# Performance work log

Hardware: AMD Instinct MI355X
Metric: run time of the kernel (lower is better)

## Reference

```python
import jax, jax.numpy as jnp
import numpy as np

B, P, G = 16, 16000, 256          # images, RPN proposals, gt boxes per image
S = 512                           # batch_size_per_image
POS_FRAC = 0.25
FG_T, BG_T = 0.5, 0.5             # fg/bg IoU thresholds
NUM_CLASSES = 91
BOX_W = jnp.array([10.0, 10.0, 5.0, 5.0], jnp.float32)  # box_coder weights
BETA = 1.0 / 9.0                  # smooth_l1 beta


def _make_boxes(k, n, img=800.0, maxwh=200.0):
    k1, k2 = jax.random.split(k)
    xy = jax.random.uniform(k1, (B, n, 2)) * img
    wh = jax.random.uniform(k2, (B, n, 2)) * maxwh + 1.0
    return jnp.concatenate([xy, xy + wh], -1)


def setup_inputs() -> dict:
    key = jax.random.key(0)
    ks = jax.random.split(key, 6)
    proposals = _make_boxes(ks[0], P)
    gt_boxes = _make_boxes(ks[1], G)
    gt_labels = jax.random.randint(ks[2], (B, G), 1, NUM_CLASSES)
    gt_thetas = jax.random.uniform(ks[3], (B, G)) * np.pi
    class_logits = jax.random.normal(ks[4], (B * S, NUM_CLASSES))
    box_regression = jax.random.normal(ks[5], (B * S, NUM_CLASSES * 5))
    return dict(class_logits=class_logits, box_regression=box_regression,
                proposals=proposals, gt_boxes=gt_boxes,
                gt_thetas=gt_thetas, gt_labels=gt_labels)


def _box_iou(a, b):
    # a: [G,4] gt, b: [M,4] proposals -> [G,M]
    area_a = (a[:, 2] - a[:, 0]) * (a[:, 3] - a[:, 1])
    area_b = (b[:, 2] - b[:, 0]) * (b[:, 3] - b[:, 1])
    lt = jnp.maximum(a[:, None, :2], b[None, :, :2])
    rb = jnp.minimum(a[:, None, 2:], b[None, :, 2:])
    wh = jnp.clip(rb - lt, 0.0)
    inter = wh[..., 0] * wh[..., 1]
    return inter / (area_a[:, None] + area_b[None, :] - inter)


def _encode(ref, prop):
    pw = prop[:, 2] - prop[:, 0]; ph = prop[:, 3] - prop[:, 1]
    px = prop[:, 0] + 0.5 * pw;   py = prop[:, 1] + 0.5 * ph
    gw = ref[:, 2] - ref[:, 0];   gh = ref[:, 3] - ref[:, 1]
    gx = ref[:, 0] + 0.5 * gw;    gy = ref[:, 1] + 0.5 * gh
    t = jnp.stack([(gx - px) / pw, (gy - py) / ph,
                   jnp.log(gw / pw), jnp.log(gh / ph)], 1)
    return t * BOX_W[None, :]


def _select_training_samples(props, gtb, gtl, gtt):
    # add_gt_proposals
    props_all = jnp.concatenate([props, gtb], 0)        # [P+G,4]
    # assign_targets_to_proposals (Matcher, allow_low_quality=False)
    iou = _box_iou(gtb, props_all)                      # [G,P+G]
    vals = iou.max(0)
    matches = iou.argmax(0)                             # clamped matched idxs
    below = vals < BG_T
    between = (vals >= BG_T) & (vals < FG_T)
    lbl = gtl[matches]
    lbl = jnp.where(below, 0, lbl)      # background
    lbl = jnp.where(between, -1, lbl)   # ignored
    # BalancedPositiveNegativeSampler (deterministic first-k variant)
    pos = lbl > 0
    neg = lbl == 0
    n_pos = jnp.minimum(pos.sum(), int(S * POS_FRAC))
    sel_pos = pos & (jnp.cumsum(pos) <= n_pos)
    sel_neg = neg & (jnp.cumsum(neg) <= (S - n_pos))
    mask = sel_pos | sel_neg
    sampled = jnp.argsort((~mask).astype(jnp.int32), stable=True)[:S]  # sorted selected idxs
    props_s = props_all[sampled]
    lbl_s = lbl[sampled]
    m = matches[sampled]
    reg = _encode(gtb[m], props_s)                       # [S,4]
    reg_t = jnp.concatenate([reg, gtt[m][:, None]], 1)   # append theta -> [S,5]
    return lbl_s, reg_t


def _fastrcnn_loss(class_logits, box_regression, labels, reg_targets):
    N = class_logits.shape[0]
    logp = jax.nn.log_softmax(class_logits, -1)
    cls_loss = -jnp.take_along_axis(logp, labels[:, None], 1).mean()
    br = box_regression.reshape(N, -1, 5)
    idx = jnp.broadcast_to(labels[:, None, None], (N, 1, 5))
    pred = jnp.take_along_axis(br, idx, axis=1)[:, 0, :]
    d = pred - reg_targets
    ad = jnp.abs(d)
    sl1 = jnp.where(ad < BETA, 0.5 * d * d / BETA, ad - 0.5 * BETA)
    pos = (labels > 0).astype(sl1.dtype)
    box_loss = jnp.sum(sl1 * pos[:, None]) / N
    return jnp.stack([cls_loss, box_loss])


def reference(class_logits, box_regression, proposals, gt_boxes, gt_thetas, gt_labels):
    labels, reg_t = jax.vmap(_select_training_samples)(proposals, gt_boxes, gt_labels, gt_thetas)
    labels = labels.reshape(-1)
    reg_t = reg_t.reshape(-1, 5)
    return _fastrcnn_loss(class_logits, box_regression, labels, reg_t)
```

## Files before the change

### kernel.cpp

```cpp
#include <hip/hip_runtime.h>

#define NB 16
#define NP 16000
#define NG 256
#define NM (NP + NG)
#define NSTRIP 254
#define NS 512
#define NCLS 91
#define SL1_BETA (1.0f/9.0f)
#define MATCHX 64
#define STATSX 4

__global__ __launch_bounds__(256) void k1_kernel(
    const float4* __restrict__ props4,
    const float4* __restrict__ gt4,
    const int*    __restrict__ gt_labels,
    const float*  __restrict__ logits,
    unsigned int* __restrict__ posinfo,
    float*        __restrict__ stats)
{
    const int b    = blockIdx.y;
    const int bx   = blockIdx.x;
    const int tid  = threadIdx.x;
    const int lane = tid & 63;
    const int wid  = tid >> 6;

    if (bx >= MATCHX) {
        const int sid = (bx - MATCHX) * NB + b;
        for (int rr = 0; rr < 32; ++rr) {
            const int r = sid * 128 + wid * 32 + rr;
            const float* row = logits + (size_t)r * NCLS;
            float a = (lane < NCLS)      ? row[lane]      : -3.0e38f;
            float c = (lane + 64 < NCLS) ? row[lane + 64] : -3.0e38f;
            float mx = fmaxf(a, c);
            #pragma unroll
            for (int o = 32; o; o >>= 1) mx = fmaxf(mx, __shfl_xor(mx, o, 64));
            float ss = 0.0f;
            if (lane < NCLS)      ss += expf(a - mx);
            if (lane + 64 < NCLS) ss += expf(c - mx);
            #pragma unroll
            for (int o = 32; o; o >>= 1) ss += __shfl_xor(ss, o, 64);
            if (lane == 0) stats[r] = mx + logf(ss);
        }
        return;
    }

    __shared__ float4 gbox[NG];
    __shared__ float  gar[NG];

    {
        const float4 v = gt4[(size_t)b * NG + tid];
        gbox[tid] = v;
        gar[tid]  = (v.z - v.x) * (v.w - v.y);
    }
    __syncthreads();

    const int j = bx * 256 + tid;
    if (j >= NM) return;

    const float4 pb = (j < NP) ? props4[(size_t)b * NP + j]
                               : gt4[(size_t)b * NG + (j - NP)];
    const float ap = (pb.z - pb.x) * (pb.w - pb.y);

    unsigned qm[8];
    int qcnt = 0, gf = 0;
    #pragma unroll
    for (int w = 0; w < 8; ++w) {
        unsigned m = 0;
        #pragma unroll
        for (int t = 0; t < 32; ++t) {
            const int g = w * 32 + t;
            const float4 gb = gbox[g];
            const float  ga = gar[g];
            float lx = fmaxf(gb.x, pb.x), ly = fmaxf(gb.y, pb.y);
            float rx = fminf(gb.z, pb.z), ry = fminf(gb.w, pb.w);
            float ww = fmaxf(rx - lx, 0.0f), hh = fmaxf(ry - ly, 0.0f);
            float inter = ww * hh;
            float tt = ga + ap;
            if (fmaf(inter, 3.0f, -tt) >= 0.0f) m |= (1u << t);
        }
        qm[w] = m;
        if (qcnt == 0 && m) gf = w * 32 + (__ffs(m) - 1);
        qcnt += __popc(m);
    }

    unsigned info = 0;
    if (qcnt > 0) {
        int gstar = gf;
        if (qcnt > 1) {
            float ib = -1.0f, ub = 1.0f; gstar = 0;
            #pragma unroll
            for (int w = 0; w < 8; ++w) {
                unsigned m = qm[w];
                while (m) {
                    int t = __ffs(m) - 1; m &= m - 1;
                    int g = w * 32 + t;
                    const float4 gb = gbox[g];
                    float lx = fmaxf(gb.x, pb.x), ly = fmaxf(gb.y, pb.y);
                    float rx = fminf(gb.z, pb.z), ry = fminf(gb.w, pb.w);
                    float ww = fmaxf(rx - lx, 0.0f), hh = fmaxf(ry - ly, 0.0f);
                    float inter = ww * hh;
                    float u = (gar[g] + ap) - inter;
                    if (inter * ub > ib * u) { ib = inter; ub = u; gstar = g; }
                }
            }
        }
        info = ((unsigned)gstar << 16) | (unsigned)gt_labels[b * NG + gstar];
    }
    posinfo[(size_t)b * NM + j] = info;
}

__global__ __launch_bounds__(256) void k2_kernel(
    const float4* __restrict__ props4,
    const float4* __restrict__ gt4,
    const float*  __restrict__ gt_thetas,
    const unsigned int* __restrict__ posinfo,
    const float*  __restrict__ logits,
    const float*  __restrict__ boxreg,
    const float*  __restrict__ stats,
    float2* __restrict__ partials)
{
    __shared__ int sampled[NS];
    __shared__ int wsum[4];

    const int b    = blockIdx.x;
    const int tid  = threadIdx.x;
    const int lane = tid & 63;
    const int wid  = tid >> 6;
    const unsigned* P = posinfo + (size_t)b * NM;
    const int base = tid * 64;

    unsigned long long pm = 0ull;
    int cn = 0;
    if (tid < NSTRIP) {
        const uint4* Pv = reinterpret_cast<const uint4*>(P + base);
        #pragma unroll
        for (int q = 0; q < 16; ++q) {
            uint4 v = Pv[q];
            int e = q * 4;
            if (v.x) pm |= 1ull << (e + 0);
            if (v.y) pm |= 1ull << (e + 1);
            if (v.z) pm |= 1ull << (e + 2);
            if (v.w) pm |= 1ull << (e + 3);
        }
        cn = 64 - __popcll(pm);
    }
    int cp = (tid < NSTRIP) ? __popcll(pm) : 0;
    int val  = (cp << 16) | cn;
    int incl = val;
    #pragma unroll
    for (int off = 1; off < 64; off <<= 1) {
        int u = __shfl_up(incl, off, 64);
        if (lane >= off) incl += u;
    }
    if (lane == 63) wsum[wid] = incl;
    __syncthreads();
    int wbase = 0;
    #pragma unroll
    for (int w = 0; w < 4; ++w) if (w < wid) wbase += wsum[w];
    int tot  = wsum[0] + wsum[1] + wsum[2] + wsum[3];
    int excl = wbase + incl - val;
    int rp = excl >> 16, rn = excl & 0xffff;
    int posT = tot >> 16, negT = tot & 0xffff;
    int np = posT < 128 ? posT : 128;
    int nn = NS - np; if (nn > negT) nn = negT;

    if (tid < NSTRIP) {
        #pragma unroll 4
        for (int e = 0; e < 64; ++e) {
            int idx = base + e;
            if ((pm >> e) & 1ull) {
                if (rp < np) sampled[rp + (rn < nn ? rn : nn)] = idx;
                rp++;
            } else {
                if (rn < nn) sampled[rn + (rp < np ? rp : np)] = idx;
                rn++;
            }
        }
    }
    __syncthreads();
    if (tid == 0 && np + nn < NS) {
        int cpp = 0, cnn = 0, i = np + nn;
        for (int idx = 0; idx < NM && i < NS; ++idx) {
            bool p = P[idx] != 0;
            bool sel;
            if (p) { sel = cpp < np; cpp++; } else { sel = cnn < nn; cnn++; }
            if (!sel) sampled[i++] = idx;
        }
    }
    __syncthreads();

    float cls_acc = 0.0f, box_acc = 0.0f;
    #pragma unroll
    for (int it = 0; it < 2; ++it) {
        const int i = tid + it * 256;
        const int r = b * NS + i;
        const int idx = sampled[i];
        const unsigned info = P[idx];
        int lbl = 0;
        if (info) lbl = info & 0xffff;
        cls_acc += stats[r] - logits[(size_t)r * NCLS + lbl];
        if (info) {
            const int m = info >> 16;
            float4 pv = (idx < NP) ? props4[(size_t)b * NP + idx]
                                   : gt4[(size_t)b * NG + (idx - NP)];
            float4 rv = gt4[(size_t)b * NG + m];
            float pw = pv.z - pv.x, ph = pv.w - pv.y;
            float px = pv.x + 0.5f * pw, py = pv.y + 0.5f * ph;
            float gw = rv.z - rv.x, gh = rv.w - rv.y;
            float gx = rv.x + 0.5f * gw, gy = rv.y + 0.5f * gh;
            float o0 = 10.0f * (gx - px) / pw;
            float o1 = 10.0f * (gy - py) / ph;
            float o2 = 5.0f * logf(gw / pw);
            float o3 = 5.0f * logf(gh / ph);
            float o4 = gt_thetas[b * NG + m];
            const float* pr = boxreg + (size_t)r * (NCLS * 5) + lbl * 5;
            float tg[5] = { o0, o1, o2, o3, o4 };
            #pragma unroll
            for (int k = 0; k < 5; ++k) {
                float d  = pr[k] - tg[k];
                float ad = fabsf(d);
                box_acc += (ad < SL1_BETA) ? 0.5f * d * d / SL1_BETA
                                           : ad - 0.5f * SL1_BETA;
            }
        }
    }
    #pragma unroll
    for (int o = 32; o; o >>= 1) {
        cls_acc += __shfl_xor(cls_acc, o, 64);
        box_acc += __shfl_xor(box_acc, o, 64);
    }
    __shared__ float cc[4], bb[4];
    if (lane == 0) { cc[wid] = cls_acc; bb[wid] = box_acc; }
    __syncthreads();
    if (tid == 0)
        partials[b] = make_float2(cc[0] + cc[1] + cc[2] + cc[3],
                                  bb[0] + bb[1] + bb[2] + bb[3]);
}

__global__ void final_kernel(const float2* __restrict__ partials,
                             float* __restrict__ out)
{
    const int tid = threadIdx.x;
    float2 v = (tid < NB) ? partials[tid] : make_float2(0.f, 0.f);
    float c = v.x, bx = v.y;
    #pragma unroll
    for (int o = 32; o; o >>= 1) {
        c  += __shfl_xor(c, o, 64);
        bx += __shfl_xor(bx, o, 64);
    }
    if (tid == 0) {
        const float invN = 1.0f / (float)(NB * NS);
        out[0] = c * invN;
        out[1] = bx * invN;
    }
}

extern "C" void kernel_launch(void* const* d_in, const int* in_sizes, int n_in,
                              void* d_out, int out_size, void* d_ws, size_t ws_size,
                              hipStream_t stream)
{
    const float* class_logits   = (const float*)d_in[0];
    const float* box_regression = (const float*)d_in[1];
    const float4* props4        = (const float4*)d_in[2];
    const float4* gt4           = (const float4*)d_in[3];
    const float* gt_thetas      = (const float*)d_in[4];
    const int*   gt_labels      = (const int*)d_in[5];
    float* out = (float*)d_out;

    char* ws = (char*)d_ws;
    unsigned int* posinfo = (unsigned int*)ws;
    char* pend = ws + (((size_t)NB * NM * 4 + 255) & ~255ull);
    float* stats = (float*)pend;
    float2* partials = (float2*)(pend + (((size_t)NB * NS * 4 + 255) & ~255ull));

    hipLaunchKernelGGL(k1_kernel, dim3(MATCHX + STATSX, NB), dim3(256), 0, stream,
                       props4, gt4, gt_labels, class_logits, posinfo, stats);
    hipLaunchKernelGGL(k2_kernel, dim3(NB), dim3(256), 0, stream,
                       props4, gt4, gt_thetas, posinfo, class_logits,
                       box_regression, stats, partials);
    hipLaunchKernelGGL(final_kernel, dim3(1), dim3(64), 0, stream, partials, out);
}
```

Baseline: 60.29 us.

## Process two proposals per thread in IoU matching to reuse gt box loads

Each thread in the matching kernel now handles two proposals (A and B), so each gt box read from LDS is shared by two IoU evaluations. The grid shrinks by half (MATCHX 64->32). The gt area is recomputed inline instead of kept in a shared array, and the inner loop goes from full unroll to unroll 4. This is meant to cut LDS traffic and block count per proposal, at the cost of more registers, possible lower occupancy, and fewer blocks to spread across CUs.

```diff
diff --git a/kernel.cpp b/kernel.cpp
--- a/kernel.cpp
+++ b/kernel.cpp
@@ -8,7 +8,7 @@
 #define NS 512
 #define NCLS 91
 #define SL1_BETA (1.0f/9.0f)
-#define MATCHX 64
+#define MATCHX 32
 #define STATSX 4
 
 __global__ __launch_bounds__(256) void k1_kernel(
@@ -46,68 +46,108 @@
     }
 
     __shared__ float4 gbox[NG];
-    __shared__ float  gar[NG];
-
-    {
-        const float4 v = gt4[(size_t)b * NG + tid];
-        gbox[tid] = v;
-        gar[tid]  = (v.z - v.x) * (v.w - v.y);
-    }
-    __syncthreads();
-
-    const int j = bx * 256 + tid;
-    if (j >= NM) return;
-
-    const float4 pb = (j < NP) ? props4[(size_t)b * NP + j]
-                               : gt4[(size_t)b * NG + (j - NP)];
-    const float ap = (pb.z - pb.x) * (pb.w - pb.y);
-
-    unsigned qm[8];
-    int qcnt = 0, gf = 0;
+
+    gbox[tid] = gt4[(size_t)b * NG + tid];
+    __syncthreads();
+
+    const int jA = bx * 512 + tid;
+    const int jB = jA + 256;
+    const bool vB = (jB < NM);
+
+    const float4 pA = (jA < NP) ? props4[(size_t)b * NP + jA] : gbox[jA - NP];
+    float4 pB = make_float4(0.f, 0.f, 0.f, 0.f);
+    if (vB) pB = (jB < NP) ? props4[(size_t)b * NP + jB] : gbox[jB - NP];
+    const float apA = (pA.z - pA.x) * (pA.w - pA.y);
+    const float apB = (pB.z - pB.x) * (pB.w - pB.y);
+
+    unsigned qmA[8], qmB[8];
+    int qcA = 0, qcB = 0, gfA = 0, gfB = 0;
     #pragma unroll
     for (int w = 0; w < 8; ++w) {
-        unsigned m = 0;
-        #pragma unroll
+        unsigned mA = 0, mB = 0;
+        #pragma unroll 4
         for (int t = 0; t < 32; ++t) {
-            const int g = w * 32 + t;
-            const float4 gb = gbox[g];
-            const float  ga = gar[g];
-            float lx = fmaxf(gb.x, pb.x), ly = fmaxf(gb.y, pb.y);
-            float rx = fminf(gb.z, pb.z), ry = fminf(gb.w, pb.w);
-            float ww = fmaxf(rx - lx, 0.0f), hh = fmaxf(ry - ly, 0.0f);
-            float inter = ww * hh;
-            float tt = ga + ap;
-            if (fmaf(inter, 3.0f, -tt) >= 0.0f) m |= (1u << t);
-        }
-        qm[w] = m;
-        if (qcnt == 0 && m) gf = w * 32 + (__ffs(m) - 1);
-        qcnt += __popc(m);
-    }
-
-    unsigned info = 0;
-    if (qcnt > 0) {
-        int gstar = gf;
-        if (qcnt > 1) {
+            const float4 gb = gbox[w * 32 + t];
+            const float  ga = (gb.z - gb.x) * (gb.w - gb.y);
+            {
+                float lx = fmaxf(gb.x, pA.x), ly = fmaxf(gb.y, pA.y);
+                float rx = fminf(gb.z, pA.z), ry = fminf(gb.w, pA.w);
+                float ww = fmaxf(rx - lx, 0.0f), hh = fmaxf(ry - ly, 0.0f);
+                float inter = ww * hh;
+                float tt = ga + apA;
+                if (fmaf(inter, 3.0f, -tt) >= 0.0f) mA |= (1u << t);
+            }
+            {
+                float lx = fmaxf(gb.x, pB.x), ly = fmaxf(gb.y, pB.y);
+                float rx = fminf(gb.z, pB.z), ry = fminf(gb.w, pB.w);
+                float ww = fmaxf(rx - lx, 0.0f), hh = fmaxf(ry - ly, 0.0f);
+                float inter = ww * hh;
+                float tt = ga + apB;
+                if (fmaf(inter, 3.0f, -tt) >= 0.0f) mB |= (1u << t);
+            }
+        }
+        qmA[w] = mA; qmB[w] = mB;
+        if (qcA == 0 && mA) gfA = w * 32 + (__ffs(mA) - 1);
+        if (qcB == 0 && mB) gfB = w * 32 + (__ffs(mB) - 1);
+        qcA += __popc(mA);
+        qcB += __popc(mB);
+    }
+
+    if (qcA > 0) {
+        int gstar = gfA;
+        if (qcA > 1) {
             float ib = -1.0f, ub = 1.0f; gstar = 0;
             #pragma unroll
             for (int w = 0; w < 8; ++w) {
-                unsigned m = qm[w];
+                unsigned m = qmA[w];
                 while (m) {
                     int t = __ffs(m) - 1; m &= m - 1;
                     int g = w * 32 + t;
                     const float4 gb = gbox[g];
-                    float lx = fmaxf(gb.x, pb.x), ly = fmaxf(gb.y, pb.y);
-                    float rx = fminf(gb.z, pb.z), ry = fminf(gb.w, pb.w);
+                    float lx = fmaxf(gb.x, pA.x), ly = fmaxf(gb.y, pA.y);
+                    float rx = fminf(gb.z, pA.z), ry = fminf(gb.w, pA.w);
                     float ww = fmaxf(rx - lx, 0.0f), hh = fmaxf(ry - ly, 0.0f);
                     float inter = ww * hh;
-                    float u = (gar[g] + ap) - inter;
+                    float ga = (gb.z - gb.x) * (gb.w - gb.y);
+                    float u  = (ga + apA) - inter;
                     if (inter * ub > ib * u) { ib = inter; ub = u; gstar = g; }
                 }
             }
         }
-        info = ((unsigned)gstar << 16) | (unsigned)gt_labels[b * NG + gstar];
-    }
-    posinfo[(size_t)b * NM + j] = info;
+        posinfo[(size_t)b * NM + jA] =
+            ((unsigned)gstar << 16) | (unsigned)gt_labels[b * NG + gstar];
+    } else {
+        posinfo[(size_t)b * NM + jA] = 0;
+    }
+
+    if (vB) {
+        if (qcB > 0) {
+            int gstar = gfB;
+            if (qcB > 1) {
+                float ib = -1.0f, ub = 1.0f; gstar = 0;
+                #pragma unroll
+                for (int w = 0; w < 8; ++w) {
+                    unsigned m = qmB[w];
+                    while (m) {
+                        int t = __ffs(m) - 1; m &= m - 1;
+                        int g = w * 32 + t;
+                        const float4 gb = gbox[g];
+                        float lx = fmaxf(gb.x, pB.x), ly = fmaxf(gb.y, pB.y);
+                        float rx = fminf(gb.z, pB.z), ry = fminf(gb.w, pB.w);
+                        float ww = fmaxf(rx - lx, 0.0f), hh = fmaxf(ry - ly, 0.0f);
+                        float inter = ww * hh;
+                        float ga = (gb.z - gb.x) * (gb.w - gb.y);
+                        float u  = (ga + apB) - inter;
+                        if (inter * ub > ib * u) { ib = inter; ub = u; gstar = g; }
+                    }
+                }
+            }
+            posinfo[(size_t)b * NM + jB] =
+                ((unsigned)gstar << 16) | (unsigned)gt_labels[b * NG + gstar];
+        } else {
+            posinfo[(size_t)b * NM + jB] = 0;
+        }
+    }
 }
 
 __global__ __launch_bounds__(256) void k2_kernel(
@@ -209,13 +249,13 @@
             float px = pv.x + 0.5f * pw, py = pv.y + 0.5f * ph;
             float gw = rv.z - rv.x, gh = rv.w - rv.y;
             float gx = rv.x + 0.5f * gw, gy = rv.y + 0.5f * gh;
-            float o0 = 10.0f * (gx - px) / pw;
-            float o1 = 10.0f * (gy - py) / ph;
-            float o2 = 5.0f * logf(gw / pw);
-            float o3 = 5.0f * logf(gh / ph);
-            float o4 = gt_thetas[b * NG + m];
+            float tg[5];
+            tg[0] = 10.0f * (gx - px) / pw;
+            tg[1] = 10.0f * (gy - py) / ph;
+            tg[2] = 5.0f * logf(gw / pw);
+            tg[3] = 5.0f * logf(gh / ph);
+            tg[4] = gt_thetas[b * NG + m];
             const float* pr = boxreg + (size_t)r * (NCLS * 5) + lbl * 5;
-            float tg[5] = { o0, o1, o2, o3, o4 };
             #pragma unroll
             for (int k = 0; k < 5; ++k) {
                 float d  = pr[k] - tg[k];
```

Result: slower. 67.13 us (+11.4%).
